# Kernel optimization log

Hardware: AMD Instinct MI355X
Metric: run time of the kernel (lower is better)

The kernel has to match this reference:

```python
import jax, jax.numpy as jnp
import numpy as np

L, E, H, C, N = 3, 512, 8, 64, 65536
DH = E // H
LN_EPS = 1e-5


def setup_inputs() -> dict:
    key = jax.random.key(0)
    ks = jax.random.split(key, 10)
    s = 1.0 / np.sqrt(E)
    return {
        "support_features": jax.random.normal(ks[0], (N, E), jnp.float32),
        "support_labels": jax.random.randint(ks[1], (N,), 0, C),
        "W1": jax.random.normal(ks[2], (L, E, E), jnp.float32) * s,
        "b1": jnp.zeros((L, E), jnp.float32),
        "gamma": jnp.ones((L, E), jnp.float32),
        "beta": jnp.zeros((L, E), jnp.float32),
        "W2": jax.random.normal(ks[3], (L, E, E), jnp.float32) * s,
        "b2": jnp.zeros((L, E), jnp.float32),
        "Wq": jax.random.normal(ks[4], (E, E), jnp.float32) * s,
        "bq": jnp.zeros((E,), jnp.float32),
        "Wk": jax.random.normal(ks[5], (E, E), jnp.float32) * s,
        "bk": jnp.zeros((E,), jnp.float32),
        "Wv": jax.random.normal(ks[6], (E, E), jnp.float32) * s,
        "bv": jnp.zeros((E,), jnp.float32),
        "Wo": jax.random.normal(ks[7], (E, E), jnp.float32) * s,
        "bo": jnp.zeros((E,), jnp.float32),
        "level_weights": jnp.ones((L,), jnp.float32) / L,
        "level_temps": jnp.ones((L,), jnp.float32),
    }


def _layer_norm(x, g, b):
    mu = jnp.mean(x, axis=-1, keepdims=True)
    var = jnp.var(x, axis=-1, keepdims=True)
    return (x - mu) * jax.lax.rsqrt(var + LN_EPS) * g + b


def reference(support_features, support_labels, W1, b1, gamma, beta, W2, b2,
              Wq, bq, Wk, bk, Wv, bv, Wo, bo, level_weights, level_temps):
    # class membership mask [C, N]; segment counts [C]
    onehot = support_labels[None, :] == jnp.arange(C)[:, None]
    counts = jnp.sum(onehot, axis=1).astype(support_features.dtype)
    scale = 1.0 / np.sqrt(DH)
    protos = []
    for l in range(L):  # small fixed number of levels
        # prototype MLP (dropout inactive at eval)
        h = jnp.maximum(_layer_norm(support_features @ W1[l] + b1[l], gamma[l], beta[l]), 0.0)
        feat = h @ W2[l] + b2[l]                              # [N, E]
        # per-class mean context (segment mean) -> query
        ctx = (onehot.astype(feat.dtype) @ feat) / counts[:, None]  # [C, E]
        q = (ctx @ Wq + bq).reshape(C, H, DH)
        k = (feat @ Wk + bk).reshape(N, H, DH)
        v = (feat @ Wv + bv).reshape(N, H, DH)
        scores = jnp.einsum('chd,nhd->chn', q, k) * scale      # [C, H, N]
        scores = jnp.where(onehot[:, None, :], scores, -jnp.inf)
        attn = jax.nn.softmax(scores, axis=-1)
        out = jnp.einsum('chn,nhd->chd', attn, v).reshape(C, E)
        protos.append(out @ Wo + bo)                           # [C, E]
    lw = jax.nn.softmax(level_weights)
    final = protos[0] * (lw[0] / level_temps[0])
    for i in range(1, L):
        final = final + protos[i] * (lw[i] / level_temps[i])
    return final
```

## Files before the change

### kernel.cpp

```cpp
#include <hip/hip_runtime.h>
#include <math.h>

#define N_SUP 65536
#define E_DIM 512
#define H_HEADS 8
#define C_CLS 64
#define DHD 64
#define L_LEV 3
#define LN_EPS 1e-5f
#define ATTN_SPLITS 8
#define CTX_SPLITS 16
#define SCAT_BLOCKS 256
#define KV_LD 1024

typedef _Float16 f16x8 __attribute__((ext_vector_type(8)));
typedef _Float16 f16x4 __attribute__((ext_vector_type(4)));
typedef float f32x4 __attribute__((ext_vector_type(4)));

__device__ __forceinline__ void gload_lds16(const void* g, void* lds) {
    __builtin_amdgcn_global_load_lds((const __attribute__((address_space(1))) void*)g,
                                     (__attribute__((address_space(3))) void*)lds,
                                     16, 0, 0);
}

__global__ __launch_bounds__(512, 2)
void hgemm256(const _Float16* __restrict__ A, int lda, size_t aStride,
              const _Float16* __restrict__ Bt, size_t btStride,
              const float* __restrict__ bias, size_t biasStride,
              _Float16* __restrict__ C, int ldc, size_t cStride, int nCol) {
    const int z = blockIdx.y;
    A += z * aStride; Bt += z * btStride; bias += z * biasStride; C += z * cStride;

    const int nRow = gridDim.x / nCol;
    const int R = nRow < 64 ? nRow : 64;
    const int bid = blockIdx.x;
    const int bandSz = R * nCol;
    const int band = bid / bandSz;
    const int rem = bid % bandSz;
    const int colT = rem / R;
    const int rowT = band * R + (rem % R);
    const int row0 = rowT * 256, col0 = colT * 256;

    __shared__ _Float16 smem[2][2][256][64];

    const int tid = threadIdx.x;
    const int wave = tid >> 6, lane = tid & 63;
    const int wm2 = (wave & 1) * 128;
    const int wn4 = (wave >> 1) * 64;
    const int m = lane & 15, q = lane >> 4;

    const int sr = tid >> 3;
    const int sb = tid & 7;
    const int sblk = sb ^ (sr & 7);

    const _Float16* Asrc = A + (size_t)(row0 + sr) * lda + sblk * 8;
    const _Float16* Bsrc = Bt + (size_t)(col0 + sr) * E_DIM + sblk * 8;
    const size_t aPass = (size_t)64 * lda;
    const size_t bPass = (size_t)64 * E_DIM;

#define SLOTA(T) ((char*)&smem[(T) & 1][0][0][0] + wave * 1024)
#define SLOTB(T) ((char*)&smem[(T) & 1][1][0][0] + wave * 1024)
#define STAGE_A(T, p) gload_lds16(Asrc + (size_t)(p) * aPass + (T) * 64, SLOTA(T) + (p) * 8192)
#define STAGE_B(T, p) gload_lds16(Bsrc + (size_t)(p) * bPass + (T) * 64, SLOTB(T) + (p) * 8192)

    f32x4 acc[8][4];
#pragma unroll
    for (int i = 0; i < 8; ++i)
#pragma unroll
        for (int j = 0; j < 4; ++j) acc[i][j] = (f32x4){0.f, 0.f, 0.f, 0.f};

    const int c0k = ((q) ^ (m & 7)) * 8;
    const int c1k = ((4 + q) ^ (m & 7)) * 8;

    STAGE_B(0, 0); STAGE_B(0, 1); STAGE_B(0, 2); STAGE_B(0, 3);
    STAGE_A(0, 0); STAGE_A(0, 2); STAGE_A(0, 1); STAGE_A(0, 3);
    STAGE_B(1, 0); STAGE_B(1, 1); STAGE_B(1, 2); STAGE_B(1, 3);
    STAGE_A(1, 0); STAGE_A(1, 2);
    asm volatile("s_waitcnt vmcnt(6)" ::: "memory");
    __builtin_amdgcn_s_barrier();

    for (int t = 0; t < 8; ++t) {
        const _Float16* As = &smem[t & 1][0][0][0];
        const _Float16* Bs = &smem[t & 1][1][0][0];
        f16x8 b0[4], b1[4];
        f16x8 a0[2], a1[2];

#pragma unroll
        for (int fc = 0; fc < 4; ++fc) {
            const int rb = (wn4 + fc * 16 + m) * 64;
            b0[fc] = *(const f16x8*)&Bs[rb + c0k];
            b1[fc] = *(const f16x8*)&Bs[rb + c1k];
        }
#pragma unroll
        for (int i = 0; i < 2; ++i) {
            const int rb = (wm2 + i * 16 + m) * 64;
            a0[i] = *(const f16x8*)&As[rb + c0k];
            a1[i] = *(const f16x8*)&As[rb + c1k];
        }
        if (t < 7) { STAGE_A(t + 1, 1); STAGE_A(t + 1, 3); }
        __builtin_amdgcn_s_barrier();
        asm volatile("s_waitcnt lgkmcnt(0)" ::: "memory");
        __builtin_amdgcn_s_setprio(1);
#pragma unroll
        for (int i = 0; i < 2; ++i)
#pragma unroll
            for (int fc = 0; fc < 4; ++fc) {
                acc[i][fc] = __builtin_amdgcn_mfma_f32_16x16x32_f16(a0[i], b0[fc], acc[i][fc], 0, 0, 0);
                acc[i][fc] = __builtin_amdgcn_mfma_f32_16x16x32_f16(a1[i], b1[fc], acc[i][fc], 0, 0, 0);
            }
        __builtin_amdgcn_s_setprio(0);
        __builtin_amdgcn_s_barrier();

#pragma unroll
        for (int p = 1; p < 4; ++p) {
#pragma unroll
            for (int i = 0; i < 2; ++i) {
                const int rb = (wm2 + (2 * p + i) * 16 + m) * 64;
                a0[i] = *(const f16x8*)&As[rb + c0k];
                a1[i] = *(const f16x8*)&As[rb + c1k];
            }
            if (p == 1) { if (t < 6) { STAGE_B(t + 2, 0); STAGE_B(t + 2, 1); } }
            if (p == 2) { if (t < 6) { STAGE_B(t + 2, 2); STAGE_B(t + 2, 3); } }
            if (p == 3) { if (t < 6) { STAGE_A(t + 2, 0); STAGE_A(t + 2, 2); } }
            __builtin_amdgcn_s_barrier();
            asm volatile("s_waitcnt lgkmcnt(0)" ::: "memory");
            __builtin_amdgcn_s_setprio(1);
#pragma unroll
            for (int i = 0; i < 2; ++i)
#pragma unroll
                for (int fc = 0; fc < 4; ++fc) {
                    acc[2 * p + i][fc] = __builtin_amdgcn_mfma_f32_16x16x32_f16(a0[i], b0[fc], acc[2 * p + i][fc], 0, 0, 0);
                    acc[2 * p + i][fc] = __builtin_amdgcn_mfma_f32_16x16x32_f16(a1[i], b1[fc], acc[2 * p + i][fc], 0, 0, 0);
                }
            __builtin_amdgcn_s_setprio(0);
            if (p == 3) {
                if (t < 6)       asm volatile("s_waitcnt vmcnt(6)" ::: "memory");
                else if (t == 6) asm volatile("s_waitcnt vmcnt(0)" ::: "memory");
            }
            __builtin_amdgcn_s_barrier();
        }
    }
#undef STAGE_A
#undef STAGE_B
#undef SLOTA
#undef SLOTB

#pragma unroll
    for (int fr = 0; fr < 8; ++fr) {
        const int rbase = row0 + wm2 + fr * 16 + q * 4;
#pragma unroll
        for (int fc = 0; fc < 4; ++fc) {
            const int col = col0 + wn4 + fc * 16 + m;
            const float bv = bias[col];
#pragma unroll
            for (int r = 0; r < 4; ++r)
                C[(size_t)(rbase + r) * ldc + col] = (_Float16)(acc[fr][fc][r] + bv);
        }
    }
}

__global__ __launch_bounds__(256)
void conv32to16(const float* __restrict__ in, _Float16* __restrict__ out, int n4) {
    int i = blockIdx.x * 256 + threadIdx.x;
    if (i < n4) {
        f32x4 v = ((const f32x4*)in)[i];
        f16x4 o = {(_Float16)v[0], (_Float16)v[1], (_Float16)v[2], (_Float16)v[3]};
        ((f16x4*)out)[i] = o;
    }
}

__global__ __launch_bounds__(256)
void transpose_all(const float* __restrict__ W1, const float* __restrict__ Wk,
                   const float* __restrict__ Wv, const float* __restrict__ Wq,
                   _Float16* __restrict__ W1allT, _Float16* __restrict__ WkvqT) {
    const int z = blockIdx.z;
    const float* src;
    _Float16* dst;
    const size_t MSZ = (size_t)E_DIM * E_DIM;
    if (z < 3)       { src = W1 + z * MSZ; dst = W1allT + z * MSZ; }
    else if (z == 3) { src = Wk;           dst = WkvqT; }
    else if (z == 4) { src = Wv;           dst = WkvqT + MSZ; }
    else             { src = Wq;           dst = WkvqT + 2 * MSZ; }

    __shared__ float t[32][33];
    const int k0 = blockIdx.x * 32, n0 = blockIdx.y * 32;
    const int tx = threadIdx.x & 31, ty = threadIdx.x >> 5;
#pragma unroll
    for (int r = 0; r < 32; r += 8)
        t[ty + r][tx] = src[(size_t)(k0 + ty + r) * E_DIM + n0 + tx];
    __syncthreads();
#pragma unroll
    for (int r = 0; r < 32; r += 8)
        dst[(size_t)(n0 + ty + r) * E_DIM + k0 + tx] = (_Float16)t[tx][ty + r];
}

__global__ __launch_bounds__(256)
void bias_compose(const float* __restrict__ b2, const float* __restrict__ Wk,
                  const float* __restrict__ Wv, const float* __restrict__ Wq,
                  const float* __restrict__ bk, const float* __restrict__ bv,
                  const float* __restrict__ bq, float* __restrict__ bcomp) {
    const int l = blockIdx.y;
    const int n = blockIdx.x * 256 + threadIdx.x;
    const float* W; const float* bb; int nn;
    if (n < 512)       { W = Wk; bb = bk; nn = n; }
    else if (n < 1024) { W = Wv; bb = bv; nn = n - 512; }
    else               { W = Wq; bb = bq; nn = n - 1024; }
    float acc = 0.f;
    for (int j = 0; j < E_DIM; ++j)
        acc = fmaf(b2[l * E_DIM + j], W[(size_t)j * E_DIM + nn], acc);
    bcomp[l * 1536 + n] = acc + bb[nn];
}

__global__ __launch_bounds__(256)
void ln_relu_all(_Float16* __restrict__ P, const float* __restrict__ gamma,
                 const float* __restrict__ beta) {
    const int row = blockIdx.x * 4 + (threadIdx.x >> 6);
    const int l = blockIdx.y;
    const int lane = threadIdx.x & 63;
    _Float16* prow = P + (size_t)row * (L_LEV * E_DIM) + l * E_DIM + lane * 8;
    const float* g = gamma + l * E_DIM + lane * 8;
    const float* b = beta  + l * E_DIM + lane * 8;
    f16x8 v = *(const f16x8*)prow;
    float x[8];
    float s = 0.f, s2 = 0.f;
#pragma unroll
    for (int e = 0; e < 8; ++e) {
        x[e] = (float)v[e];
        s += x[e];
        s2 = fmaf(x[e], x[e], s2);
    }
#pragma unroll
    for (int off = 32; off; off >>= 1) {
        s  += __shfl_xor(s, off);
        s2 += __shfl_xor(s2, off);
    }
    const float mean = s * (1.f / E_DIM);
    const float var  = s2 * (1.f / E_DIM) - mean * mean;
    const float rstd = rsqrtf(var + LN_EPS);
    f32x4 g0 = *(const f32x4*)g;
    f32x4 g1 = *(const f32x4*)(g + 4);
    f32x4 b0 = *(const f32x4*)b;
    f32x4 b1 = *(const f32x4*)(b + 4);
    f16x8 o;
#pragma unroll
    for (int e = 0; e < 4; ++e) {
        o[e]     = (_Float16)fmaxf(fmaf((x[e]     - mean) * rstd, g0[e], b0[e]), 0.f);
        o[e + 4] = (_Float16)fmaxf(fmaf((x[e + 4] - mean) * rstd, g1[e], b1[e]), 0.f);
    }
    *(f16x8*)prow = o;
}

__global__ __launch_bounds__(256)
void label_block_hist(const int* __restrict__ labels, int* __restrict__ blockCounts) {
    __shared__ int h[C_CLS];
    const int tid = threadIdx.x;
    if (tid < C_CLS) h[tid] = 0;
    __syncthreads();
    atomicAdd(&h[labels[blockIdx.x * 256 + tid]], 1);
    __syncthreads();
    if (tid < C_CLS) blockCounts[blockIdx.x * C_CLS + tid] = h[tid];
}

__global__ __launch_bounds__(64)
void scan_offsets(const int* __restrict__ blockCounts, int* __restrict__ counts,
                  int* __restrict__ offs, int* __restrict__ blockOffs) {
    const int c = threadIdx.x;
    int total = 0;
    for (int b = 0; b < SCAT_BLOCKS; ++b) total += blockCounts[b * C_CLS + c];
    counts[c] = total;
    __shared__ int tot[C_CLS];
    tot[c] = total;
    __syncthreads();
    int off = 0;
    for (int cc = 0; cc < c; ++cc) off += tot[cc];
    offs[c] = off;
    if (c == C_CLS - 1) offs[C_CLS] = off + total;
    int run = off;
    for (int b = 0; b < SCAT_BLOCKS; ++b) {
        blockOffs[b * C_CLS + c] = run;
        run += blockCounts[b * C_CLS + c];
    }
}

__global__ __launch_bounds__(256)
void scatter_sorted(const int* __restrict__ labels, const int* __restrict__ blockOffs,
                    int* __restrict__ members) {
    __shared__ int cur[C_CLS];
    const int tid = threadIdx.x;
    if (tid < C_CLS) cur[tid] = blockOffs[blockIdx.x * C_CLS + tid];
    __syncthreads();
    const int i = blockIdx.x * 256 + tid;
    const int c = labels[i];
    const int p = atomicAdd(&cur[c], 1);
    members[p] = i;
}

__global__ __launch_bounds__(256)
void zero_f32(float* __restrict__ p, int n) {
    int i = blockIdx.x * 256 + threadIdx.x;
    if (i < n) p[i] = 0.f;
}

__global__ __launch_bounds__(256)
void ctx_partial(const _Float16* __restrict__ P, const int* __restrict__ members,
                 const int* __restrict__ offsets, float* __restrict__ hpart) {
    const int c = blockIdx.x, split = blockIdx.y, l = blockIdx.z;
    const _Float16* src = P + (size_t)l * E_DIM;
    const int tid = threadIdx.x;
    const int wave = tid >> 6, lane = tid & 63;
    const int start = offsets[c], end = offsets[c + 1];
    const int wg = split * 4 + wave;
    const int stride = 4 * CTX_SPLITS;
    const int ld = L_LEV * E_DIM;

    float acc[8];
#pragma unroll
    for (int e = 0; e < 8; ++e) acc[e] = 0.f;

    int i = start + wg;
    for (; i + stride < end; i += 2 * stride) {
        const int n0 = members[i];
        const int n1 = members[i + stride];
        f16x8 r0 = *(const f16x8*)(src + (size_t)n0 * ld + lane * 8);
        f16x8 r1 = *(const f16x8*)(src + (size_t)n1 * ld + lane * 8);
#pragma unroll
        for (int e = 0; e < 8; ++e) acc[e] += (float)r0[e] + (float)r1[e];
    }
    if (i < end) {
        const int n0 = members[i];
        f16x8 r0 = *(const f16x8*)(src + (size_t)n0 * ld + lane * 8);
#pragma unroll
        for (int e = 0; e < 8; ++e) acc[e] += (float)r0[e];
    }

    __shared__ float red[4][64][8];
#pragma unroll
    for (int e = 0; e < 8; ++e) red[wave][lane][e] = acc[e];
    __syncthreads();
    float* dst = hpart + (((size_t)l * C_CLS + c) * CTX_SPLITS + split) * E_DIM;
#pragma unroll
    for (int t = 0; t < 2; ++t) {
        const int col = tid * 2 + t;
        const int ln = col >> 3, e = col & 7;
        dst[col] = red[0][ln][e] + red[1][ln][e] + red[2][ln][e] + red[3][ln][e];
    }
}

__global__ __launch_bounds__(256)
void row_gemm_q(const float* __restrict__ hpart, const int* __restrict__ counts,
                const _Float16* __restrict__ W2compT, const float* __restrict__ bcomp,
                float* __restrict__ q) {
    const int c = blockIdx.x, l = blockIdx.y;
    const int tid = threadIdx.x;
    const float inv = 1.f / (float)counts[c];
    __shared__ float xrow[E_DIM];
    const float* hp = hpart + ((size_t)l * C_CLS + c) * CTX_SPLITS * E_DIM;
    float s0 = 0.f, s1 = 0.f;
#pragma unroll
    for (int s = 0; s < CTX_SPLITS; ++s) {
        s0 += hp[s * E_DIM + tid];
        s1 += hp[s * E_DIM + tid + 256];
    }
    xrow[tid]       = s0 * inv;
    xrow[tid + 256] = s1 * inv;
    __syncthreads();

    const _Float16* Wq = W2compT + (size_t)l * 1536 * E_DIM + (size_t)1024 * E_DIM;
    const float* bias = bcomp + l * 1536 + 1024;
    const int n0 = tid, n1 = tid + 256;
    float a0 = 0.f, a1 = 0.f;
#pragma unroll 4
    for (int k0 = 0; k0 < E_DIM; k0 += 8) {
        f16x8 w0 = *(const f16x8*)(Wq + (size_t)n0 * E_DIM + k0);
        f16x8 w1 = *(const f16x8*)(Wq + (size_t)n1 * E_DIM + k0);
#pragma unroll
        for (int e = 0; e < 8; ++e) {
            const float xv = xrow[k0 + e];
            a0 = fmaf(xv, (float)w0[e], a0);
            a1 = fmaf(xv, (float)w1[e], a1);
        }
    }
    float* qq = q + (size_t)l * C_CLS * E_DIM;
    qq[c * E_DIM + n0] = a0 + bias[n0];
    qq[c * E_DIM + n1] = a1 + bias[n1];
}

__global__ __launch_bounds__(256)
void attn_partial(const float* __restrict__ q, const _Float16* __restrict__ kv,
                  const int* __restrict__ members, const int* __restrict__ offsets,
                  float* __restrict__ pm, float* __restrict__ pl,
                  float* __restrict__ po) {
    const int c = blockIdx.x, h = blockIdx.y, s = blockIdx.z;
    const int tid = threadIdx.x;
    const int wave = tid >> 6, lane = tid & 63;
    const int start = offsets[c], end = offsets[c + 1];
    const int g = s * 4 + wave;

    float qv[64];
    const bool active = (start + g * 64) < end;
    if (active) {
        const float* qrow = q + c * E_DIM + h * DHD;
#pragma unroll
        for (int d = 0; d < 64; ++d) qv[d] = qrow[d];
    }

    __shared__ float ps[4][64];
    float m = -INFINITY, lsum = 0.f, out = 0.f;

    for (int ch0 = start + g * 64; ch0 < end; ch0 += 4 * ATTN_SPLITS * 64) {
        const int nvalid = min(64, end - ch0);
        const int idx = ch0 + lane;
        const int mi = members[idx < end ? idx : end - 1];
        const _Float16* krow = kv + (size_t)mi * KV_LD + h * DHD;
        float dot = 0.f;
#pragma unroll
        for (int j = 0; j < 8; ++j) {
            f16x8 kr = *(const f16x8*)(krow + j * 8);
#pragma unroll
            for (int e = 0; e < 8; ++e)
                dot = fmaf((float)kr[e], qv[j * 8 + e], dot);
        }
        float sc = (lane < nvalid) ? dot * 0.125f : -INFINITY;
        float cm = sc;
#pragma unroll
        for (int off = 32; off; off >>= 1) cm = fmaxf(cm, __shfl_xor(cm, off));
        const float nm = fmaxf(m, cm);
        const float alpha = __expf(m - nm);
        const float p = (lane < nvalid) ? __expf(sc - nm) : 0.f;
        ps[wave][lane] = p;
        out *= alpha;
        lsum *= alpha;
        m = nm;
        asm volatile("" ::: "memory");
#pragma unroll 16
        for (int j = 0; j < 64; ++j) {
            const int nj = __shfl(mi, j);
            const float pj = ps[wave][j];
            const float vv = (float)kv[(size_t)nj * KV_LD + E_DIM + h * DHD + lane];
            out = fmaf(pj, vv, out);
            lsum += pj;
        }
    }

    __shared__ float rm[4], rl[4], racc[4][64];
    racc[wave][lane] = out;
    if (lane == 0) { rm[wave] = m; rl[wave] = lsum; }
    __syncthreads();
    if (wave == 0) {
        float M = fmaxf(fmaxf(rm[0], rm[1]), fmaxf(rm[2], rm[3]));
        float o = 0.f, Lt = 0.f;
#pragma unroll
        for (int w = 0; w < 4; ++w) {
            const float al = (rm[w] > -INFINITY) ? __expf(rm[w] - M) : 0.f;
            o  += al * racc[w][lane];
            Lt += al * rl[w];
        }
        const int pidx = (c * H_HEADS + h) * ATTN_SPLITS + s;
        po[pidx * 64 + lane] = o;
        if (lane == 0) { pm[pidx] = M; pl[pidx] = Lt; }
    }
}

__global__ __launch_bounds__(256)
void proto_accum(const float* __restrict__ pm, const float* __restrict__ pl,
                 const float* __restrict__ po, const float* __restrict__ Wo,
                 const float* __restrict__ bo, const float* __restrict__ lvlw,
                 const float* __restrict__ lvlt, int l, float* __restrict__ out) {
    const int c = blockIdx.x;
    const int tid = threadIdx.x;
    const int wave = tid >> 6, lane = tid & 63;
    __shared__ float xrow[E_DIM];
#pragma unroll
    for (int hh = wave; hh < H_HEADS; hh += 4) {
        const int ch = c * H_HEADS + hh;
        float M = -INFINITY;
#pragma unroll
        for (int s = 0; s < ATTN_SPLITS; ++s) M = fmaxf(M, pm[ch * ATTN_SPLITS + s]);
        float o = 0.f, Lt = 0.f;
#pragma unroll
        for (int s = 0; s < ATTN_SPLITS; ++s) {
            const int pidx = ch * ATTN_SPLITS + s;
            const float al = (pm[pidx] > -INFINITY) ? __expf(pm[pidx] - M) : 0.f;
            o  += al * po[pidx * 64 + lane];
            Lt += al * pl[pidx];
        }
        xrow[hh * 64 + lane] = o / Lt;
    }
    __syncthreads();

    float a0 = 0.f, a1 = 0.f;
#pragma unroll 8
    for (int k = 0; k < E_DIM; ++k) {
        float cv = xrow[k];
        a0 = fmaf(cv, Wo[(size_t)k * E_DIM + tid], a0);
        a1 = fmaf(cv, Wo[(size_t)k * E_DIM + tid + 256], a1);
    }
    float w0 = lvlw[0], w1 = lvlw[1], w2 = lvlw[2];
    float mx = fmaxf(w0, fmaxf(w1, w2));
    float e0 = expf(w0 - mx), e1 = expf(w1 - mx), e2 = expf(w2 - mx);
    float ssum = e0 + e1 + e2;
    float lw = (l == 0 ? e0 : (l == 1 ? e1 : e2)) / ssum;
    float coef = lw / lvlt[l];
    float r0 = (a0 + bo[tid]) * coef;
    float r1 = (a1 + bo[tid + 256]) * coef;
    if (l == 0) {
        out[c * E_DIM + tid]       = r0;
        out[c * E_DIM + tid + 256] = r1;
    } else {
        out[c * E_DIM + tid]       += r0;
        out[c * E_DIM + tid + 256] += r1;
    }
}

extern "C" void kernel_launch(void* const* d_in, const int* in_sizes, int n_in,
                              void* d_out, int out_size, void* d_ws, size_t ws_size,
                              hipStream_t stream) {
    const float* X      = (const float*)d_in[0];
    const int*   labels = (const int*)  d_in[1];
    const float* W1     = (const float*)d_in[2];
    const float* b1     = (const float*)d_in[3];
    const float* gamma  = (const float*)d_in[4];
    const float* beta   = (const float*)d_in[5];
    const float* W2     = (const float*)d_in[6];
    const float* b2     = (const float*)d_in[7];
    const float* Wq     = (const float*)d_in[8];
    const float* bq     = (const float*)d_in[9];
    const float* Wk     = (const float*)d_in[10];
    const float* bk     = (const float*)d_in[11];
    const float* Wv     = (const float*)d_in[12];
    const float* bv     = (const float*)d_in[13];
    const float* Wo     = (const float*)d_in[14];
    const float* bo     = (const float*)d_in[15];
    const float* lvlw   = (const float*)d_in[16];
    const float* lvlt   = (const float*)d_in[17];
    float* out = (float*)d_out;

    char* p = (char*)d_ws;
    const size_t MSZ = (size_t)E_DIM * E_DIM;
    _Float16* Xh      = (_Float16*)p; p += (size_t)N_SUP * E_DIM * 2;
    _Float16* bufPall = (_Float16*)p; p += (size_t)N_SUP * E_DIM * L_LEV * 2;
    _Float16* bufKV   = (_Float16*)p; p += (size_t)N_SUP * KV_LD * 2;
    _Float16* W1allT  = (_Float16*)p; p += L_LEV * MSZ * 2;
    _Float16* WkvqT   = (_Float16*)p; p += 3 * MSZ * 2;
    _Float16* W2f16   = (_Float16*)p; p += L_LEV * MSZ * 2;
    _Float16* W2compT = (_Float16*)p; p += (size_t)L_LEV * 1536 * E_DIM * 2;
    float* zeros512 = (float*)p; p += E_DIM * sizeof(float);
    float* bcomp = (float*)p; p += L_LEV * 1536 * sizeof(float);
    float* hpart = (float*)p; p += (size_t)L_LEV * C_CLS * CTX_SPLITS * E_DIM * sizeof(float);
    float* qb    = (float*)p; p += (size_t)L_LEV * C_CLS * E_DIM * sizeof(float);
    float* pm    = (float*)p; p += C_CLS * H_HEADS * ATTN_SPLITS * sizeof(float);
    float* pl    = (float*)p; p += C_CLS * H_HEADS * ATTN_SPLITS * sizeof(float);
    float* po    = (float*)p; p += (size_t)C_CLS * H_HEADS * ATTN_SPLITS * 64 * sizeof(float);
    int* counts      = (int*)p; p += 256;
    int* offs        = (int*)p; p += 512;
    int* members     = (int*)p; p += (size_t)N_SUP * sizeof(int);
    int* blockCounts = (int*)p; p += (size_t)SCAT_BLOCKS * C_CLS * sizeof(int);
    int* blockOffs   = (int*)p; p += (size_t)SCAT_BLOCKS * C_CLS * sizeof(int);

    label_block_hist<<<SCAT_BLOCKS, 256, 0, stream>>>(labels, blockCounts);
    scan_offsets<<<1, 64, 0, stream>>>(blockCounts, counts, offs, blockOffs);
    scatter_sorted<<<SCAT_BLOCKS, 256, 0, stream>>>(labels, blockOffs, members);

    conv32to16<<<(N_SUP * E_DIM / 4) / 256, 256, 0, stream>>>(X, Xh, N_SUP * E_DIM / 4);
    conv32to16<<<(int)(L_LEV * MSZ / 4 / 256), 256, 0, stream>>>(W2, W2f16, L_LEV * MSZ / 4);
    transpose_all<<<dim3(16, 16, 6), 256, 0, stream>>>(W1, Wk, Wv, Wq, W1allT, WkvqT);
    zero_f32<<<2, 256, 0, stream>>>(zeros512, E_DIM);

    hgemm256<<<dim3(6 * 2, L_LEV), 512, 0, stream>>>(
        WkvqT, E_DIM, 0, W2f16, MSZ, zeros512, 0,
        W2compT, E_DIM, (size_t)1536 * E_DIM, 2);
    bias_compose<<<dim3(6, L_LEV), 256, 0, stream>>>(b2, Wk, Wv, Wq, bk, bv, bq, bcomp);

    const int nRowT = N_SUP / 256;
    hgemm256<<<dim3(nRowT * 6, 1), 512, 0, stream>>>(
        Xh, E_DIM, 0, W1allT, 0, b1, 0, bufPall, L_LEV * E_DIM, 0, 6);
    ln_relu_all<<<dim3(N_SUP / 4, L_LEV), 256, 0, stream>>>(bufPall, gamma, beta);

    ctx_partial<<<dim3(C_CLS, CTX_SPLITS, L_LEV), 256, 0, stream>>>(
        bufPall, members, offs, hpart);
    row_gemm_q<<<dim3(C_CLS, L_LEV), 256, 0, stream>>>(
        hpart, counts, W2compT, bcomp, qb);

    for (int l = 0; l < L_LEV; ++l) {
        hgemm256<<<dim3(nRowT * 4, 1), 512, 0, stream>>>(
            bufPall + (size_t)l * E_DIM, L_LEV * E_DIM, 0,
            W2compT + (size_t)l * 1536 * E_DIM, 0,
            bcomp + l * 1536, 0, bufKV, KV_LD, 0, 4);
        attn_partial<<<dim3(C_CLS, H_HEADS, ATTN_SPLITS), 256, 0, stream>>>(
            qb + (size_t)l * C_CLS * E_DIM, bufKV, members, offs, pm, pl, po);
        proto_accum<<<C_CLS, 256, 0, stream>>>(pm, pl, po, Wo, bo, lvlw, lvlt, l, out);
    }
}
```

Measured before the change: 960.8 us.

## Restructure GEMM K-loop to stage whole tiles with two barriers per step

Rewrites the inner GEMM main loop schedule. The old loop had eight barriers per K-tile and interleaved partial global-to-LDS loads. The new loop splits the K=64 tile into two K halves and interleaves LDS fragment reads with MFMA groups, with only two barriers per iteration. The whole next-next tile is issued at once after the first barrier. This cuts synchronisation overhead and lets LDS reads overlap with MFMAs, at the cost of higher register pressure from 16 A fragments and burstier global loads.

```diff
diff --git a/kernel.cpp b/kernel.cpp
--- a/kernel.cpp
+++ b/kernel.cpp
@@ -62,6 +62,11 @@
 #define SLOTB(T) ((char*)&smem[(T) & 1][1][0][0] + wave * 1024)
 #define STAGE_A(T, p) gload_lds16(Asrc + (size_t)(p) * aPass + (T) * 64, SLOTA(T) + (p) * 8192)
 #define STAGE_B(T, p) gload_lds16(Bsrc + (size_t)(p) * bPass + (T) * 64, SLOTB(T) + (p) * 8192)
+#define STAGE_TILE(T)                                                         \
+    {                                                                         \
+        STAGE_B(T, 0); STAGE_B(T, 1); STAGE_B(T, 2); STAGE_B(T, 3);           \
+        STAGE_A(T, 0); STAGE_A(T, 1); STAGE_A(T, 2); STAGE_A(T, 3);           \
+    }
 
     f32x4 acc[8][4];
 #pragma unroll
@@ -72,74 +77,80 @@
     const int c0k = ((q) ^ (m & 7)) * 8;
     const int c1k = ((4 + q) ^ (m & 7)) * 8;
 
-    STAGE_B(0, 0); STAGE_B(0, 1); STAGE_B(0, 2); STAGE_B(0, 3);
-    STAGE_A(0, 0); STAGE_A(0, 2); STAGE_A(0, 1); STAGE_A(0, 3);
-    STAGE_B(1, 0); STAGE_B(1, 1); STAGE_B(1, 2); STAGE_B(1, 3);
-    STAGE_A(1, 0); STAGE_A(1, 2);
-    asm volatile("s_waitcnt vmcnt(6)" ::: "memory");
+    STAGE_TILE(0);
+    STAGE_TILE(1);
+    asm volatile("s_waitcnt vmcnt(8)" ::: "memory");
     __builtin_amdgcn_s_barrier();
 
     for (int t = 0; t < 8; ++t) {
         const _Float16* As = &smem[t & 1][0][0][0];
         const _Float16* Bs = &smem[t & 1][1][0][0];
         f16x8 b0[4], b1[4];
-        f16x8 a0[2], a1[2];
-
-#pragma unroll
-        for (int fc = 0; fc < 4; ++fc) {
-            const int rb = (wn4 + fc * 16 + m) * 64;
-            b0[fc] = *(const f16x8*)&Bs[rb + c0k];
-            b1[fc] = *(const f16x8*)&Bs[rb + c1k];
-        }
-#pragma unroll
-        for (int i = 0; i < 2; ++i) {
-            const int rb = (wm2 + i * 16 + m) * 64;
-            a0[i] = *(const f16x8*)&As[rb + c0k];
-            a1[i] = *(const f16x8*)&As[rb + c1k];
-        }
-        if (t < 7) { STAGE_A(t + 1, 1); STAGE_A(t + 1, 3); }
+        f16x8 aA[4], aB[4], aC[4], aD[4];
+
+#pragma unroll
+        for (int fc = 0; fc < 4; ++fc)
+            b0[fc] = *(const f16x8*)&Bs[(wn4 + fc * 16 + m) * 64 + c0k];
+#pragma unroll
+        for (int i = 0; i < 4; ++i)
+            aA[i] = *(const f16x8*)&As[(wm2 + i * 16 + m) * 64 + c0k];
+#pragma unroll
+        for (int i = 0; i < 4; ++i)
+            aB[i] = *(const f16x8*)&As[(wm2 + (4 + i) * 16 + m) * 64 + c0k];
+
+        __builtin_amdgcn_s_setprio(1);
+#pragma unroll
+        for (int i = 0; i < 4; ++i)
+#pragma unroll
+            for (int fc = 0; fc < 4; ++fc)
+                acc[i][fc] = __builtin_amdgcn_mfma_f32_16x16x32_f16(aA[i], b0[fc], acc[i][fc], 0, 0, 0);
+        __builtin_amdgcn_s_setprio(0);
+
+#pragma unroll
+        for (int fc = 0; fc < 4; ++fc)
+            b1[fc] = *(const f16x8*)&Bs[(wn4 + fc * 16 + m) * 64 + c1k];
+#pragma unroll
+        for (int i = 0; i < 4; ++i)
+            aC[i] = *(const f16x8*)&As[(wm2 + i * 16 + m) * 64 + c1k];
+
+        __builtin_amdgcn_s_setprio(1);
+#pragma unroll
+        for (int i = 0; i < 4; ++i)
+#pragma unroll
+            for (int fc = 0; fc < 4; ++fc)
+                acc[4 + i][fc] = __builtin_amdgcn_mfma_f32_16x16x32_f16(aB[i], b0[fc], acc[4 + i][fc], 0, 0, 0);
+        __builtin_amdgcn_s_setprio(0);
+
+#pragma unroll
+        for (int i = 0; i < 4; ++i)
+            aD[i] = *(const f16x8*)&As[(wm2 + (4 + i) * 16 + m) * 64 + c1k];
+
+        __builtin_amdgcn_s_setprio(1);
+#pragma unroll
+        for (int i = 0; i < 4; ++i)
+#pragma unroll
+            for (int fc = 0; fc < 4; ++fc)
+                acc[i][fc] = __builtin_amdgcn_mfma_f32_16x16x32_f16(aC[i], b1[fc], acc[i][fc], 0, 0, 0);
+        __builtin_amdgcn_s_setprio(0);
+
+        asm volatile("s_waitcnt lgkmcnt(0)" ::: "memory");
         __builtin_amdgcn_s_barrier();
-        asm volatile("s_waitcnt lgkmcnt(0)" ::: "memory");
+
+        if (t < 6) STAGE_TILE(t + 2);
+
         __builtin_amdgcn_s_setprio(1);
 #pragma unroll
-        for (int i = 0; i < 2; ++i)
-#pragma unroll
-            for (int fc = 0; fc < 4; ++fc) {
-                acc[i][fc] = __builtin_amdgcn_mfma_f32_16x16x32_f16(a0[i], b0[fc], acc[i][fc], 0, 0, 0);
-                acc[i][fc] = __builtin_amdgcn_mfma_f32_16x16x32_f16(a1[i], b1[fc], acc[i][fc], 0, 0, 0);
-            }
+        for (int i = 0; i < 4; ++i)
+#pragma unroll
+            for (int fc = 0; fc < 4; ++fc)
+                acc[4 + i][fc] = __builtin_amdgcn_mfma_f32_16x16x32_f16(aD[i], b1[fc], acc[4 + i][fc], 0, 0, 0);
         __builtin_amdgcn_s_setprio(0);
+
+        if (t < 6)       asm volatile("s_waitcnt vmcnt(8)" ::: "memory");
+        else if (t == 6) asm volatile("s_waitcnt vmcnt(0)" ::: "memory");
         __builtin_amdgcn_s_barrier();
-
-#pragma unroll
-        for (int p = 1; p < 4; ++p) {
-#pragma unroll
-            for (int i = 0; i < 2; ++i) {
-                const int rb = (wm2 + (2 * p + i) * 16 + m) * 64;
-                a0[i] = *(const f16x8*)&As[rb + c0k];
-                a1[i] = *(const f16x8*)&As[rb + c1k];
-            }
-            if (p == 1) { if (t < 6) { STAGE_B(t + 2, 0); STAGE_B(t + 2, 1); } }
-            if (p == 2) { if (t < 6) { STAGE_B(t + 2, 2); STAGE_B(t + 2, 3); } }
-            if (p == 3) { if (t < 6) { STAGE_A(t + 2, 0); STAGE_A(t + 2, 2); } }
-            __builtin_amdgcn_s_barrier();
-            asm volatile("s_waitcnt lgkmcnt(0)" ::: "memory");
-            __builtin_amdgcn_s_setprio(1);
-#pragma unroll
-            for (int i = 0; i < 2; ++i)
-#pragma unroll
-                for (int fc = 0; fc < 4; ++fc) {
-                    acc[2 * p + i][fc] = __builtin_amdgcn_mfma_f32_16x16x32_f16(a0[i], b0[fc], acc[2 * p + i][fc], 0, 0, 0);
-                    acc[2 * p + i][fc] = __builtin_amdgcn_mfma_f32_16x16x32_f16(a1[i], b1[fc], acc[2 * p + i][fc], 0, 0, 0);
-                }
-            __builtin_amdgcn_s_setprio(0);
-            if (p == 3) {
-                if (t < 6)       asm volatile("s_waitcnt vmcnt(6)" ::: "memory");
-                else if (t == 6) asm volatile("s_waitcnt vmcnt(0)" ::: "memory");
-            }
-            __builtin_amdgcn_s_barrier();
-        }
-    }
+    }
+#undef STAGE_TILE
 #undef STAGE_A
 #undef STAGE_B
 #undef SLOTA
```

After: 954.3 us. About the same (-0.7%).
